# Kernel optimization log

Measured on AMD Instinct MI355X. Metric: run time of the kernel, lower is better.

## Reference

```python
import jax, jax.numpy as jnp
import numpy as np

N, B, M, K, C = 120000, 8, 60000, 16, 32
EX = 512  # 128 * expansion_factor 4
EPS = 1e-5


def _bn(h, g, b):
    # BatchNorm1d (training-mode batch stats, biased var), stats over points
    m = h.mean(axis=0)
    v = h.var(axis=0)
    return (h - m) * jax.lax.rsqrt(v + EPS) * g + b


def setup_inputs() -> dict:
    key = jax.random.key(0)
    ks = jax.random.split(key, 20)

    def w(i, shape, fan):
        return jax.random.normal(ks[i], shape, jnp.float32) / np.sqrt(fan)

    inp = {}
    inp["x"] = jax.random.normal(ks[0], (N, C), jnp.float32)
    inp["pos"] = jax.random.normal(ks[1], (N, 3), jnp.float32) * 5.0
    inp["batch"] = jnp.sort(jax.random.randint(ks[2], (N,), 0, B))
    inp["reflectance"] = jax.random.uniform(ks[3], (N,), jnp.float32)
    inp["sf"] = jax.random.uniform(ks[4], (B,), jnp.float32, minval=0.5, maxval=1.5)
    inp["idx"] = jnp.sort(jax.random.randint(ks[5], (M,), 0, N))
    inp["edge_src"] = jax.random.randint(ks[6], (M * K,), 0, N)
    inp["edge_dst"] = jnp.repeat(jnp.arange(M), K)
    # local_nn MLP channels [C+4, 64, 64, 128]; first layer has no BN
    inp["mlp_W1"] = w(7, (C + 4, 64), C + 4); inp["mlp_b1"] = jnp.zeros((64,))
    inp["mlp_W2"] = w(8, (64, 64), 64); inp["mlp_b2"] = jnp.zeros((64,))
    inp["mlp_g2"] = jnp.ones((64,)); inp["mlp_be2"] = jnp.zeros((64,))
    inp["mlp_W3"] = w(9, (64, 128), 64); inp["mlp_b3"] = jnp.zeros((128,))
    inp["mlp_g3"] = jnp.ones((128,)); inp["mlp_be3"] = jnp.zeros((128,))
    # ReflectanceYesNo (1 -> 32 -> 32 -> 1)
    inp["ryn_W1"] = w(10, (1, 32), 1); inp["ryn_b1"] = jnp.zeros((32,))
    inp["ryn_W2"] = w(11, (32, 32), 32); inp["ryn_b2"] = jnp.zeros((32,))
    inp["ryn_W3"] = w(12, (32, 1), 32); inp["ryn_b3"] = jnp.zeros((1,))
    # InvertedResidualBlock 128 -> 512 -> 128 (all 1x1 convs)
    inp["exp_W"] = w(13, (128, EX), 128); inp["exp_b"] = jnp.zeros((EX,))
    inp["exp_g"] = jnp.ones((EX,)); inp["exp_be"] = jnp.zeros((EX,))
    inp["dw_w"] = jax.random.normal(ks[14], (2, EX), jnp.float32)  # depthwise k=1 -> per-channel scale
    inp["dw_b"] = jnp.zeros((2, EX)); inp["dw_g"] = jnp.ones((2, EX)); inp["dw_be"] = jnp.zeros((2, EX))
    inp["pw_W"] = w(15, (2, EX, EX), EX); inp["pw_b"] = jnp.zeros((2, EX))
    inp["pw_g"] = jnp.ones((2, EX)); inp["pw_be"] = jnp.zeros((2, EX))
    inp["c_g"] = jnp.ones((2, EX)); inp["c_be"] = jnp.zeros((2, EX))
    inp["proj_W"] = w(16, (EX, 128), EX); inp["proj_b"] = jnp.zeros((128,))
    inp["proj_g"] = jnp.ones((128,)); inp["proj_be"] = jnp.zeros((128,))
    return inp


def reference(x, pos, batch, reflectance, sf, idx, edge_src, edge_dst,
              mlp_W1, mlp_b1, mlp_W2, mlp_b2, mlp_g2, mlp_be2, mlp_W3, mlp_b3, mlp_g3, mlp_be3,
              ryn_W1, ryn_b1, ryn_W2, ryn_b2, ryn_W3, ryn_b3,
              exp_W, exp_b, exp_g, exp_be, dw_w, dw_b, dw_g, dw_be,
              pw_W, pw_b, pw_g, pw_be, c_g, c_be, proj_W, proj_b, proj_g, proj_be):
    Bn = sf.shape[0]
    Mn = idx.shape[0]
    pos4 = jnp.concatenate([pos[:, :3], reflectance[:, None]], axis=-1)  # [N,4]

    # --- ReflectanceYesNo gating (gumbel_softmax over a size-1 axis == ones, straight-through) ---
    h = jax.nn.relu(reflectance[:, None] @ ryn_W1 + ryn_b1)
    h = jax.nn.relu(h @ ryn_W2 + ryn_b2)
    pooled = jax.ops.segment_sum(h, batch, num_segments=Bn)
    counts = jax.ops.segment_sum(jnp.ones((h.shape[0],), h.dtype), batch, num_segments=Bn)
    logits = (pooled / counts[:, None]) @ ryn_W3 + ryn_b3  # [B,1]
    y_soft = jax.nn.softmax(logits, axis=-1)               # size-1 softmax -> all ones
    y = jax.lax.stop_gradient(jnp.ones_like(y_soft) - y_soft) + y_soft
    gate = jnp.where(jnp.sum(reflectance) != 0.0, y[:, 0][batch], 1.0)
    refl4 = pos4[:, 3] * gate

    # --- scale coords, PointNetConv: gather -> local_nn MLP -> max aggregate ---
    scale = sf[batch][:, None]
    pos_s = jnp.concatenate([pos4[:, :3] / scale, refl4[:, None]], axis=-1)  # [N,4]
    rel = pos_s[edge_src] - pos_s[idx][edge_dst]                              # [E,4]
    msg = jnp.concatenate([x[edge_src], rel], axis=-1)                        # [E,C+4]
    h1 = jax.nn.relu(msg @ mlp_W1 + mlp_b1)
    h2 = _bn(jax.nn.relu(h1 @ mlp_W2 + mlp_b2), mlp_g2, mlp_be2)
    h3 = _bn(jax.nn.relu(h2 @ mlp_W3 + mlp_b3), mlp_g3, mlp_be3)
    agg = jax.ops.segment_max(h3, edge_dst, num_segments=Mn)                  # [M,128]
    agg = jnp.where(jnp.isneginf(agg), 0.0, agg)  # PyG fills isolated nodes with 0

    # --- InvertedResidualBlock (1x1 convs == per-point linears, BN over points) ---
    res = agg
    e = jax.nn.relu(_bn(agg @ exp_W + exp_b, exp_g, exp_be))

    def ds(hh, i):  # DepthwiseSeparableConv1d, k=1
        d = jax.nn.relu(_bn(hh * dw_w[i] + dw_b[i], dw_g[i], dw_be[i]))
        return jax.nn.relu(_bn(d @ pw_W[i] + pw_b[i], pw_g[i], pw_be[i]))

    cmid = jax.nn.relu(_bn(ds(e, 0), c_g[0], c_be[0]))
    cmid = _bn(ds(cmid, 1), c_g[1], c_be[1])
    o = _bn(cmid @ proj_W + proj_b, proj_g, proj_be)
    out = jax.nn.relu(o + res)  # shortcut is identity (in == out channels)

    return (out, pos[idx, :3], batch[idx], reflectance[idx], sf)
```

## Files before the change

### kernel.cpp

```cpp
#include <hip/hip_runtime.h>
#include <hip/hip_bf16.h>
#include <cstdint>

#define DEV_INLINE __device__ __forceinline__

typedef unsigned short u16;
typedef unsigned int   u32;
typedef short bf16x8 __attribute__((ext_vector_type(8)));
typedef float f32x4  __attribute__((ext_vector_type(4)));

#define AS_GLOBAL(p) ((const __attribute__((address_space(1))) void*)(p))
#define AS_LDS(p)    ((__attribute__((address_space(3))) void*)(p))

constexpr int NP = 120000, NB = 8, NM = 60000, KNN = 16;
constexpr int NE = NM * KNN;
constexpr float EPS = 1e-5f;

constexpr size_t O_POS   = (size_t)NM * 128;
constexpr size_t O_BATCH = O_POS + (size_t)NM * 3;
constexpr size_t O_REFL  = O_BATCH + NM;
constexpr size_t O_SF    = O_REFL + NM;

__device__ float  g_pos_s[(size_t)NP * 4];
__device__ u16    g_xbf[(size_t)NP * 32];
__device__ u16    g_pre2[(size_t)NE * 64];
__device__ u32    g_mm[(size_t)NM * 128];
__device__ float  g_agg[(size_t)NM * 128];
__device__ u16    g_aggbf[(size_t)NM * 128];
__device__ u16    g_bufA[(size_t)NM * 512];
__device__ u16    g_bufB[(size_t)NM * 512];
__device__ float  g_obuf[(size_t)NM * 128];
__device__ float  g_sum[512], g_sqs[512], g_cfa[512], g_cfb[512];
__device__ float  g_b3adj[128], g_pbadj[128];
__device__ u16 g_w1t[64 * 64];
__device__ u16 g_w2t[64 * 64];
__device__ u16 g_w3t[128 * 64];
__device__ u16 g_expwt[512 * 128];
__device__ u16 g_pw0t[512 * 512];
__device__ u16 g_pw1t[512 * 512];
__device__ u16 g_projwt[128 * 512];

template<int ID> DEV_INLINE const u16* ubufsel() {
  if constexpr (ID == 1) return g_aggbf;
  else if constexpr (ID == 2) return g_bufA;
  else return g_bufB;
}
template<int ID> DEV_INLINE u16* obufsel() {
  if constexpr (ID == 2) return g_bufA;
  else return g_bufB;
}
template<int ID> DEV_INLINE const u16* wsel() {
  if constexpr (ID == 3) return g_expwt;
  else if constexpr (ID == 4) return g_pw0t;
  else if constexpr (ID == 5) return g_pw1t;
  else return g_projwt;
}

DEV_INLINE float bf2f(u16 u) { u32 x = (u32)u << 16; float f; __builtin_memcpy(&f, &x, 4); return f; }
DEV_INLINE u16 f2bf(float f) {
  u32 x; __builtin_memcpy(&x, &f, 4);
  return (u16)((x + 0x7FFFu + ((x >> 16) & 1u)) >> 16);
}
DEV_INLINE u32 pack2(float a, float b) { return (u32)f2bf(a) | ((u32)f2bf(b) << 16); }

__global__ void prep_pos_x(const float* __restrict__ pos, const int* __restrict__ batch,
                           const float* __restrict__ refl, const float* __restrict__ sf,
                           const float* __restrict__ x) {
  int i = blockIdx.x * blockDim.x + threadIdx.x;
  if (i >= NP) return;
  float s = sf[batch[i]];
  float4 v;
  v.x = pos[(size_t)i*3+0] / s;
  v.y = pos[(size_t)i*3+1] / s;
  v.z = pos[(size_t)i*3+2] / s;
  v.w = refl[i];
  *reinterpret_cast<float4*>(g_pos_s + (size_t)i*4) = v;
  const float4* xr = reinterpret_cast<const float4*>(x + (size_t)i*32);
#pragma unroll
  for (int q = 0; q < 4; q++) {
    float4 a = xr[q*2], b = xr[q*2+1];
    uint4 u = make_uint4(pack2(a.x,a.y), pack2(a.z,a.w), pack2(b.x,b.y), pack2(b.z,b.w));
    *reinterpret_cast<uint4*>(g_xbf + (size_t)i*32 + q*8) = u;
  }
}

__global__ void tail_out(const float* __restrict__ pos, const int* __restrict__ batch,
                         const float* __restrict__ refl, const float* __restrict__ sf,
                         const int* __restrict__ idx, float* __restrict__ out) {
  int i = blockIdx.x * blockDim.x + threadIdx.x;
  if (i < NM) {
    int p = idx[i];
    out[O_POS + (size_t)i*3+0] = pos[(size_t)p*3+0];
    out[O_POS + (size_t)i*3+1] = pos[(size_t)p*3+1];
    out[O_POS + (size_t)i*3+2] = pos[(size_t)p*3+2];
    out[O_BATCH + i] = (float)batch[p];
    out[O_REFL  + i] = refl[p];
  }
  if (i < NB) out[O_SF + i] = sf[i];
}

__global__ void zero_stats() {
  int t = threadIdx.x;
  g_sum[t] = 0.f; g_sqs[t] = 0.f;
}

__global__ void prep_weights(const float* __restrict__ W1, const float* __restrict__ W2,
                             const float* __restrict__ W3, const float* __restrict__ expW,
                             const float* __restrict__ pwW, const float* __restrict__ projW) {
  int i = blockIdx.x * 256 + threadIdx.x;
  const int s0 = 4096, s1 = 4096, s2 = 8192, s3 = 65536, s4 = 262144, s5 = 262144, s6 = 65536;
  if (i < s0) { int n = i >> 6, k = i & 63; g_w1t[i] = (k < 36) ? f2bf(W1[k*64 + n]) : (u16)0; return; }
  i -= s0;
  if (i < s1) { int n = i >> 6, k = i & 63; g_w2t[i] = f2bf(W2[k*64 + n]); return; }
  i -= s1;
  if (i < s2) { int n = i >> 6, k = i & 63; g_w3t[i] = f2bf(W3[k*128 + n]); return; }
  i -= s2;
  if (i < s3) { int n = i >> 7, k = i & 127; g_expwt[i] = f2bf(expW[k*512 + n]); return; }
  i -= s3;
  if (i < s4) { int n = i >> 9, k = i & 511; g_pw0t[i] = f2bf(pwW[k*512 + n]); return; }
  i -= s4;
  if (i < s5) { int n = i >> 9, k = i & 511; g_pw1t[i] = f2bf(pwW[262144 + k*512 + n]); return; }
  i -= s5;
  if (i < s6) { int n = i >> 9, k = i & 511; g_projwt[i] = f2bf(projW[k*128 + n]); return; }
}

__global__ void param_bn(const float* __restrict__ g, const float* __restrict__ be,
                         float n, int C) {
  int c = threadIdx.x;
  if (c < C) {
    float mean = g_sum[c] / n;
    float var  = fmaxf(g_sqs[c] / n - mean * mean, 0.f);
    float a = g[c] * rsqrtf(var + EPS);
    g_cfa[c] = a;
    g_cfb[c] = be[c] - a * mean;
  }
  __syncthreads();
  g_sum[c] = 0.f; g_sqs[c] = 0.f;
}

__global__ void param_dw(const float* __restrict__ w, const float* __restrict__ g,
                         const float* __restrict__ be, float n, int C) {
  int c = threadIdx.x;
  if (c < C) {
    float mean = g_sum[c] / n;
    float var  = fmaxf(g_sqs[c] / n - mean * mean, 0.f);
    float r = rsqrtf(w[c]*w[c]*var + EPS);
    float a = w[c] * r * g[c];
    g_cfa[c] = a;
    g_cfb[c] = be[c] - a * mean;
  }
  __syncthreads();
  g_sum[c] = 0.f; g_sqs[c] = 0.f;
}

template<int SID>
__global__ void scale_fold(const float* __restrict__ bias_in, int N, int K) {
  u16* Wt = (SID == 0) ? g_w3t : g_projwt;
  float* badj = (SID == 0) ? g_b3adj : g_pbadj;
  int w = (blockIdx.x * blockDim.x + threadIdx.x) >> 6;
  int lane = threadIdx.x & 63;
  if (w >= N) return;
  float acc = 0.f;
  for (int k = lane; k < K; k += 64) {
    float wv = bf2f(Wt[(size_t)w*K + k]);
    acc = fmaf(g_cfb[k], wv, acc);
    Wt[(size_t)w*K + k] = f2bf(g_cfa[k] * wv);
  }
#pragma unroll
  for (int o = 32; o; o >>= 1) acc += __shfl_xor(acc, o, 64);
  if (lane == 0) badj[w] = bias_in[w] + acc;
}

constexpr int K1_BLOCKS = 960;
__launch_bounds__(256)
__global__ void k1_edge(const int* __restrict__ esrc, const int* __restrict__ idx,
                        const float* __restrict__ b1v, const float* __restrict__ b2v) {
  __shared__ u16 sH[4][16][72];
  __shared__ float ssum[64], ssqs[64];
  const int tid = threadIdx.x;
  if (tid < 64) { ssum[tid] = 0.f; ssqs[tid] = 0.f; }
  __syncthreads();
  const int w = tid >> 6, lane = tid & 63, l15 = lane & 15, l4 = lane >> 4;
  u16 (*sh)[72] = sH[w];
  bf16x8 w1f[2][4], w2f[2][4];
#pragma unroll
  for (int ks = 0; ks < 2; ks++)
#pragma unroll
    for (int fc = 0; fc < 4; fc++) {
      w1f[ks][fc] = *reinterpret_cast<const bf16x8*>(g_w1t + (size_t)(fc*16+l15)*64 + ks*32 + l4*8);
      w2f[ks][fc] = *reinterpret_cast<const bf16x8*>(g_w2t + (size_t)(fc*16+l15)*64 + ks*32 + l4*8);
    }
  float b1r[4], b2r[4];
#pragma unroll
  for (int fc = 0; fc < 4; fc++) { b1r[fc] = b1v[fc*16+l15]; b2r[fc] = b2v[fc*16+l15]; }
  float s8[4] = {}, q8[4] = {};
  const int t0 = blockIdx.x * 4 + w;
  const int TSTRIDE = K1_BLOCKS * 4;
  int   s_cur = esrc[t0*16 + l15];
  uint4 x_cur = *reinterpret_cast<const uint4*>(g_xbf + (size_t)s_cur*32 + l4*8);
  float4 ps_cur = make_float4(0.f,0.f,0.f,0.f);
  if (l4 == 0) ps_cur = *reinterpret_cast<const float4*>(g_pos_s + (size_t)s_cur*4);
  float4 pc_cur = *reinterpret_cast<const float4*>(g_pos_s + (size_t)idx[t0]*4);

  for (int t = t0; t < NM; t += TSTRIDE) {
    const int tn = t + TSTRIDE;
    int s_nx = 0; uint4 x_nx = make_uint4(0,0,0,0);
    float4 ps_nx = ps_cur, pc_nx = pc_cur;
    if (tn < NM) {
      s_nx = esrc[tn*16 + l15];
      x_nx = *reinterpret_cast<const uint4*>(g_xbf + (size_t)s_nx*32 + l4*8);
      if (l4 == 0) ps_nx = *reinterpret_cast<const float4*>(g_pos_s + (size_t)s_nx*4);
      pc_nx = *reinterpret_cast<const float4*>(g_pos_s + (size_t)idx[tn]*4);
    }
    bf16x8 a0 = __builtin_bit_cast(bf16x8, x_cur);
    uint4 r4 = make_uint4(0,0,0,0);
    if (l4 == 0) {
      r4.x = pack2(ps_cur.x - pc_cur.x, ps_cur.y - pc_cur.y);
      r4.y = pack2(ps_cur.z - pc_cur.z, ps_cur.w - pc_cur.w);
    }
    bf16x8 a1 = __builtin_bit_cast(bf16x8, r4);
    f32x4 acc1[4] = {};
#pragma unroll
    for (int fc = 0; fc < 4; fc++) {
      acc1[fc] = __builtin_amdgcn_mfma_f32_16x16x32_bf16(a0, w1f[0][fc], acc1[fc], 0, 0, 0);
      acc1[fc] = __builtin_amdgcn_mfma_f32_16x16x32_bf16(a1, w1f[1][fc], acc1[fc], 0, 0, 0);
    }
#pragma unroll
    for (int fc = 0; fc < 4; fc++)
#pragma unroll
      for (int r = 0; r < 4; r++)
        sh[l4*4 + r][fc*16 + l15] = f2bf(fmaxf(acc1[fc][r] + b1r[fc], 0.f));
    bf16x8 h0  = *reinterpret_cast<const bf16x8*>(&sh[l15][l4*8]);
    bf16x8 h1v = *reinterpret_cast<const bf16x8*>(&sh[l15][32 + l4*8]);
    f32x4 acc2[4] = {};
#pragma unroll
    for (int fc = 0; fc < 4; fc++) {
      acc2[fc] = __builtin_amdgcn_mfma_f32_16x16x32_bf16(h0,  w2f[0][fc], acc2[fc], 0, 0, 0);
      acc2[fc] = __builtin_amdgcn_mfma_f32_16x16x32_bf16(h1v, w2f[1][fc], acc2[fc], 0, 0, 0);
    }
#pragma unroll
    for (int fc = 0; fc < 4; fc++)
#pragma unroll
      for (int r = 0; r < 4; r++) {
        float v = fmaxf(acc2[fc][r] + b2r[fc], 0.f);
        s8[fc] += v; q8[fc] += v*v;
        sh[l4*4 + r][fc*16 + l15] = f2bf(v);
      }
    uint4 p0 = *reinterpret_cast<const uint4*>(&sh[l15][l4*8]);
    uint4 p1 = *reinterpret_cast<const uint4*>(&sh[l15][32 + l4*8]);
    *reinterpret_cast<uint4*>(g_pre2 + (size_t)t*1024 + lane*8)       = p0;
    *reinterpret_cast<uint4*>(g_pre2 + (size_t)t*1024 + 512 + lane*8) = p1;
    s_cur = s_nx; x_cur = x_nx; ps_cur = ps_nx; pc_cur = pc_nx;
  }
#pragma unroll
  for (int fc = 0; fc < 4; fc++) {
    float sv = s8[fc], qv = q8[fc];
    sv += __shfl_xor(sv, 16, 64); sv += __shfl_xor(sv, 32, 64);
    qv += __shfl_xor(qv, 16, 64); qv += __shfl_xor(qv, 32, 64);
    if (l4 == 0) { atomicAdd(&ssum[fc*16 + l15], sv); atomicAdd(&ssqs[fc*16 + l15], qv); }
  }
  __syncthreads();
  if (tid < 64) { atomicAdd(&g_sum[tid], ssum[tid]); atomicAdd(&g_sqs[tid], ssqs[tid]); }
}

constexpr int K2_BLOCKS = 960;
__launch_bounds__(256)
__global__ void k2_edge() {
  __shared__ float ssum[128], ssqs[128];
  const int tid = threadIdx.x;
  if (tid < 128) { ssum[tid] = 0.f; ssqs[tid] = 0.f; }
  __syncthreads();
  const int lane = tid & 63, l15 = lane & 15, l4 = lane >> 4;
  const int wglobal = blockIdx.x * 4 + (tid >> 6);
  const int WSTRIDE = K2_BLOCKS * 4;
  bf16x8 w3f[2][8];
#pragma unroll
  for (int ks = 0; ks < 2; ks++)
#pragma unroll
    for (int fc = 0; fc < 8; fc++)
      w3f[ks][fc] = *reinterpret_cast<const bf16x8*>(g_w3t + (size_t)(fc*16 + l15)*64 + ks*32 + l4*8);
  float bv[8];
#pragma unroll
  for (int fc = 0; fc < 8; fc++) bv[fc] = g_b3adj[fc*16 + l15];
  float s[8] = {}, q[8] = {};
  int t = wglobal;
  uint4 an0 = make_uint4(0,0,0,0), an1 = an0;
  if (t < NM) {
    const uint4* p = reinterpret_cast<const uint4*>(g_pre2 + (size_t)t*1024 + lane*8);
    an0 = p[0]; an1 = p[64];
  }
  for (; t < NM; t += WSTRIDE) {
    uint4 a0 = an0, a1 = an1;
    int tn = t + WSTRIDE;
    if (tn < NM) {
      const uint4* p = reinterpret_cast<const uint4*>(g_pre2 + (size_t)tn*1024 + lane*8);
      an0 = p[0]; an1 = p[64];
    }
    bf16x8 af0 = __builtin_bit_cast(bf16x8, a0);
    bf16x8 af1 = __builtin_bit_cast(bf16x8, a1);
    f32x4 acc[8] = {};
#pragma unroll
    for (int fc = 0; fc < 8; fc++) {
      acc[fc] = __builtin_amdgcn_mfma_f32_16x16x32_bf16(af0, w3f[0][fc], acc[fc], 0, 0, 0);
      acc[fc] = __builtin_amdgcn_mfma_f32_16x16x32_bf16(af1, w3f[1][fc], acc[fc], 0, 0, 0);
    }
    u32 rbase = (u32)t * 128u;
#pragma unroll
    for (int fc = 0; fc < 8; fc++) {
      float v0 = fmaxf(acc[fc][0] + bv[fc], 0.f);
      float v1 = fmaxf(acc[fc][1] + bv[fc], 0.f);
      float v2 = fmaxf(acc[fc][2] + bv[fc], 0.f);
      float v3 = fmaxf(acc[fc][3] + bv[fc], 0.f);
      s[fc] += (v0 + v1) + (v2 + v3);
      q[fc] += (v0*v0 + v1*v1) + (v2*v2 + v3*v3);
      float mx = fmaxf(fmaxf(v0, v1), fmaxf(v2, v3));
      float mn = fminf(fminf(v0, v1), fminf(v2, v3));
      mx = fmaxf(mx, __shfl_xor(mx, 16, 64)); mx = fmaxf(mx, __shfl_xor(mx, 32, 64));
      mn = fminf(mn, __shfl_xor(mn, 16, 64)); mn = fminf(mn, __shfl_xor(mn, 32, 64));
      if (l4 == (fc & 3))
        g_mm[rbase + fc*16 + l15] = (u32)f2bf(mx) | ((u32)f2bf(mn) << 16);
    }
  }
#pragma unroll
  for (int fc = 0; fc < 8; fc++) {
    float sv = s[fc], qv = q[fc];
    sv += __shfl_xor(sv, 16, 64); sv += __shfl_xor(sv, 32, 64);
    qv += __shfl_xor(qv, 16, 64); qv += __shfl_xor(qv, 32, 64);
    if (l4 == 0) { atomicAdd(&ssum[fc*16 + l15], sv); atomicAdd(&ssqs[fc*16 + l15], qv); }
  }
  __syncthreads();
  if (tid < 128) { atomicAdd(&g_sum[tid], ssum[tid]); atomicAdd(&g_sqs[tid], ssqs[tid]); }
}

__global__ void k3_agg() {
  int i4 = (blockIdx.x * 256 + threadIdx.x) * 4;
  if (i4 >= NM * 128) return;
  int c = i4 & 127;
  uint4 mm = *reinterpret_cast<const uint4*>(g_mm + i4);
  float4 a = *reinterpret_cast<const float4*>(g_cfa + c);
  float4 b = *reinterpret_cast<const float4*>(g_cfb + c);
  u32 u[4] = {mm.x, mm.y, mm.z, mm.w};
  float av[4] = {a.x, a.y, a.z, a.w};
  float bb[4] = {b.x, b.y, b.z, b.w};
  float4 r;
  float* rr = &r.x;
#pragma unroll
  for (int j = 0; j < 4; j++) {
    float mx = bf2f((u16)(u[j] & 0xFFFFu));
    float mn = bf2f((u16)(u[j] >> 16));
    rr[j] = av[j] > 0.f ? fmaf(av[j], mx, bb[j]) : fmaf(av[j], mn, bb[j]);
  }
  *reinterpret_cast<float4*>(g_agg + i4) = r;
  uint2 pk; pk.x = pack2(r.x, r.y); pk.y = pack2(r.z, r.w);
  *reinterpret_cast<uint2*>(g_aggbf + i4) = pk;
}

template<int AID, int WID, int OID, int NPAN, bool OUT_BF16, bool BIAS_DEV>
__launch_bounds__(256, 3)
__global__ void gemm_mfma(const float* __restrict__ bias, int Mrows, int Kdim) {
  const int Ncols = NPAN * 128;
  const u16* __restrict__ A  = ubufsel<AID>();
  const u16* __restrict__ Bt = wsel<WID>();
  __shared__ u16 As[2][128][32];
  __shared__ u16 Bs[2][128][32];
  __shared__ float ssum[128], ssqs[128];
  const int tid = threadIdx.x;
  const int bid = blockIdx.x;
  const int m0 = (bid / NPAN) * 128, n0 = (bid % NPAN) * 128;
  if (tid < 128) { ssum[tid] = 0.f; ssqs[tid] = 0.f; }
  const int wave = tid >> 6, lane = tid & 63, l15 = lane & 15, l4 = lane >> 4;
  const int wr = wave >> 1, wc = wave & 1;
  const int ckk = (lane & 3) * 8;
  f32x4 acc[4][4] = {};
  const int nt = Kdim >> 5;

  auto STAGE = [&](int buf, int t) {
    const int k0 = t * 32;
#pragma unroll
    for (int i = 0; i < 2; i++) {
      const int c = wave * 2 + i;
      const int row = c * 16 + (lane >> 2);
      const u16* ga = A  + (size_t)(m0 + row) * Kdim + k0 + ckk;
      const u16* gb = Bt + (size_t)(n0 + row) * Kdim + k0 + ckk;
      __builtin_amdgcn_global_load_lds(AS_GLOBAL(ga), AS_LDS(&As[buf][c*16][0]), 16, 0, 0);
      __builtin_amdgcn_global_load_lds(AS_GLOBAL(gb), AS_LDS(&Bs[buf][c*16][0]), 16, 0, 0);
    }
  };

  STAGE(0, 0);
  __syncthreads();
  int cur = 0;
  for (int t = 0; t < nt; ++t) {
    if (t + 1 < nt) STAGE(cur ^ 1, t + 1);
    bf16x8 af[4], bf[4];
#pragma unroll
    for (int fr = 0; fr < 4; fr++)
      af[fr] = *reinterpret_cast<const bf16x8*>(&As[cur][wr*64 + fr*16 + l15][l4*8]);
#pragma unroll
    for (int fc = 0; fc < 4; fc++)
      bf[fc] = *reinterpret_cast<const bf16x8*>(&Bs[cur][wc*64 + fc*16 + l15][l4*8]);
#pragma unroll
    for (int fr = 0; fr < 4; fr++)
#pragma unroll
      for (int fc = 0; fc < 4; fc++)
        acc[fr][fc] = __builtin_amdgcn_mfma_f32_16x16x32_bf16(af[fr], bf[fc], acc[fr][fc], 0, 0, 0);
    if (t + 1 < nt) { __syncthreads(); cur ^= 1; }
  }

  const int orow = m0 + wr*64 + l4*4;
#pragma unroll
  for (int fc = 0; fc < 4; fc++) {
    int col = n0 + wc*64 + fc*16 + l15;
    float bvv = BIAS_DEV ? g_pbadj[col] : bias[col];
    float s = 0.f, q = 0.f;
#pragma unroll
    for (int fr = 0; fr < 4; fr++)
#pragma unroll
      for (int r = 0; r < 4; r++) {
        int row = orow + fr*16 + r;
        if (row < Mrows) {
          float v = acc[fr][fc][r] + bvv;
          s += v; q += v*v;
          if (OUT_BF16) obufsel<OID>()[(size_t)row*Ncols + col] = f2bf(v);
          else          g_obuf[(size_t)row*Ncols + col] = v;
        }
      }
    atomicAdd(&ssum[wc*64 + fc*16 + l15], s);
    atomicAdd(&ssqs[wc*64 + fc*16 + l15], q);
  }
  __syncthreads();
  if (tid < 128) { atomicAdd(&g_sum[n0 + tid], ssum[tid]); atomicAdd(&g_sqs[n0 + tid], ssqs[tid]); }
}

template<int INID, int OUTID>
__launch_bounds__(256)
__global__ void ew_stats(int rows) {
  const u16* __restrict__ X = ubufsel<INID>();
  u16* __restrict__ Y = obufsel<OUTID>();
  __shared__ float ssum[512], ssqs[512];
  const int tid = threadIdx.x;
  ssum[tid] = 0.f; ssum[tid+256] = 0.f; ssqs[tid] = 0.f; ssqs[tid+256] = 0.f;
  __syncthreads();
  const int c0 = (tid & 63) * 8;
  const int rl = tid >> 6;
  float a[8], b[8];
#pragma unroll
  for (int j = 0; j < 8; j++) { a[j] = g_cfa[c0+j]; b[j] = g_cfb[c0+j]; }
  float s[8] = {}, q[8] = {};
  for (int r = blockIdx.x*4 + rl; r < rows; r += gridDim.x*4) {
    uint4 v = *reinterpret_cast<const uint4*>(X + (size_t)r*512 + c0);
    u32 u[4] = {v.x, v.y, v.z, v.w}, o[4];
#pragma unroll
    for (int t = 0; t < 4; t++) {
      float lo = bf2f((u16)(u[t] & 0xFFFFu));
      float hi = bf2f((u16)(u[t] >> 16));
      lo = fmaxf(fmaf(a[2*t],   lo, b[2*t]),   0.f);
      hi = fmaxf(fmaf(a[2*t+1], hi, b[2*t+1]), 0.f);
      s[2*t] += lo; q[2*t] += lo*lo; s[2*t+1] += hi; q[2*t+1] += hi*hi;
      o[t] = (u32)f2bf(lo) | ((u32)f2bf(hi) << 16);
    }
    *reinterpret_cast<uint4*>(Y + (size_t)r*512 + c0) = make_uint4(o[0], o[1], o[2], o[3]);
  }
#pragma unroll
  for (int j = 0; j < 8; j++) { atomicAdd(&ssum[c0+j], s[j]); atomicAdd(&ssqs[c0+j], q[j]); }
  __syncthreads();
  atomicAdd(&g_sum[tid],     ssum[tid]);     atomicAdd(&g_sqs[tid],     ssqs[tid]);
  atomicAdd(&g_sum[tid+256], ssum[tid+256]); atomicAdd(&g_sqs[tid+256], ssqs[tid+256]);
}

template<int INID, int OUTID>
__launch_bounds__(256)
__global__ void ew_apply(int rows) {
  const u16* __restrict__ X = ubufsel<INID>();
  u16* __restrict__ Y = obufsel<OUTID>();
  const int tid = threadIdx.x;
  const int c0 = (tid & 63) * 8;
  const int rl = tid >> 6;
  float a[8], b[8];
#pragma unroll
  for (int j = 0; j < 8; j++) { a[j] = g_cfa[c0+j]; b[j] = g_cfb[c0+j]; }
  for (int r = blockIdx.x*4 + rl; r < rows; r += gridDim.x*4) {
    uint4 v = *reinterpret_cast<const uint4*>(X + (size_t)r*512 + c0);
    u32 u[4] = {v.x, v.y, v.z, v.w}, o[4];
#pragma unroll
    for (int t = 0; t < 4; t++) {
      float lo = bf2f((u16)(u[t] & 0xFFFFu));
      float hi = bf2f((u16)(u[t] >> 16));
      lo = fmaxf(fmaf(a[2*t],   lo, b[2*t]),   0.f);
      hi = fmaxf(fmaf(a[2*t+1], hi, b[2*t+1]), 0.f);
      o[t] = (u32)f2bf(lo) | ((u32)f2bf(hi) << 16);
    }
    *reinterpret_cast<uint4*>(Y + (size_t)r*512 + c0) = make_uint4(o[0], o[1], o[2], o[3]);
  }
}

__global__ void final_out(float* __restrict__ out) {
  int i4 = (blockIdx.x * 256 + threadIdx.x) * 4;
  if (i4 >= NM * 128) return;
  int c = i4 & 127;
  float4 o  = *reinterpret_cast<const float4*>(g_obuf + i4);
  float4 ag = *reinterpret_cast<const float4*>(g_agg + i4);
  float4 a  = *reinterpret_cast<const float4*>(g_cfa + c);
  float4 b  = *reinterpret_cast<const float4*>(g_cfb + c);
  float4 r;
  r.x = fmaxf(fmaf(a.x, o.x, b.x) + ag.x, 0.f);
  r.y = fmaxf(fmaf(a.y, o.y, b.y) + ag.y, 0.f);
  r.z = fmaxf(fmaf(a.z, o.z, b.z) + ag.z, 0.f);
  r.w = fmaxf(fmaf(a.w, o.w, b.w) + ag.w, 0.f);
  *reinterpret_cast<float4*>(out + i4) = r;
}

extern "C" void kernel_launch(void* const* d_in, const int* in_sizes, int n_in,
                              void* d_out, int out_size, void* d_ws, size_t ws_size,
                              hipStream_t stream) {
  const float* x     = (const float*)d_in[0];
  const float* pos   = (const float*)d_in[1];
  const int*   batch = (const int*)  d_in[2];
  const float* refl  = (const float*)d_in[3];
  const float* sf    = (const float*)d_in[4];
  const int*   idx   = (const int*)  d_in[5];
  const int*   esrc  = (const int*)  d_in[6];
  const float* W1  = (const float*)d_in[8];
  const float* b1  = (const float*)d_in[9];
  const float* W2  = (const float*)d_in[10];
  const float* b2  = (const float*)d_in[11];
  const float* g2  = (const float*)d_in[12];
  const float* be2 = (const float*)d_in[13];
  const float* W3  = (const float*)d_in[14];
  const float* b3  = (const float*)d_in[15];
  const float* g3  = (const float*)d_in[16];
  const float* be3 = (const float*)d_in[17];
  const float* expW  = (const float*)d_in[24];
  const float* expb  = (const float*)d_in[25];
  const float* expg  = (const float*)d_in[26];
  const float* expbe = (const float*)d_in[27];
  const float* dww  = (const float*)d_in[28];
  const float* dwg  = (const float*)d_in[30];
  const float* dwbe = (const float*)d_in[31];
  const float* pwW  = (const float*)d_in[32];
  const float* pwb  = (const float*)d_in[33];
  const float* pwg  = (const float*)d_in[34];
  const float* pwbe = (const float*)d_in[35];
  const float* cg   = (const float*)d_in[36];
  const float* cbe  = (const float*)d_in[37];
  const float* projW  = (const float*)d_in[38];
  const float* projb  = (const float*)d_in[39];
  const float* projg  = (const float*)d_in[40];
  const float* projbe = (const float*)d_in[41];
  float* out = (float*)d_out;

  const float fNE = (float)NE, fNM = (float)NM;

  prep_weights<<<2624, 256, 0, stream>>>(W1, W2, W3, expW, pwW, projW);
  prep_pos_x<<<(NP + 255)/256, 256, 0, stream>>>(pos, batch, refl, sf, x);
  tail_out<<<(NM + 255)/256, 256, 0, stream>>>(pos, batch, refl, sf, idx, out);
  zero_stats<<<1, 512, 0, stream>>>();

  k1_edge<<<K1_BLOCKS, 256, 0, stream>>>(esrc, idx, b1, b2);
  param_bn<<<1, 512, 0, stream>>>(g2, be2, fNE, 64);
  scale_fold<0><<<32, 256, 0, stream>>>(b3, 128, 64);
  k2_edge<<<K2_BLOCKS, 256, 0, stream>>>();
  param_bn<<<1, 512, 0, stream>>>(g3, be3, fNE, 128);
  k3_agg<<<NM*128/1024, 256, 0, stream>>>();

  gemm_mfma<1, 3, 2, 4, true, false><<<469*4, 256, 0, stream>>>(expb, NM, 128);
  param_bn<<<1, 512, 0, stream>>>(expg, expbe, fNM, 512);
  ew_stats<2, 2><<<1024, 256, 0, stream>>>(NM);
  param_dw<<<1, 512, 0, stream>>>(dww, dwg, dwbe, fNM, 512);
  ew_apply<2, 3><<<1024, 256, 0, stream>>>(NM);
  gemm_mfma<3, 4, 2, 4, true, false><<<469*4, 256, 0, stream>>>(pwb, NM, 512);
  param_bn<<<1, 512, 0, stream>>>(pwg, pwbe, fNM, 512);
  ew_stats<2, 2><<<1024, 256, 0, stream>>>(NM);
  param_bn<<<1, 512, 0, stream>>>(cg, cbe, fNM, 512);
  ew_stats<2, 2><<<1024, 256, 0, stream>>>(NM);
  param_dw<<<1, 512, 0, stream>>>(dww + 512, dwg + 512, dwbe + 512, fNM, 512);
  ew_apply<2, 3><<<1024, 256, 0, stream>>>(NM);
  gemm_mfma<3, 5, 2, 4, true, false><<<469*4, 256, 0, stream>>>(pwb + 512, NM, 512);
  param_bn<<<1, 512, 0, stream>>>(pwg + 512, pwbe + 512, fNM, 512);
  ew_stats<2, 2><<<1024, 256, 0, stream>>>(NM);
  param_bn<<<1, 512, 0, stream>>>(cg + 512, cbe + 512, fNM, 512);
  scale_fold<1><<<32, 256, 0, stream>>>(projb, 128, 512);
  gemm_mfma<2, 6, 0, 1, false, true><<<469, 256, 0, stream>>>(projb, NM, 512);
  param_bn<<<1, 512, 0, stream>>>(projg, projbe, fNM, 128);
  final_out<<<NM*128/1024, 256, 0, stream>>>(out);
}
```

Baseline: 828.0 us.

## Stage bf16 GEMM output through LDS for coalesced stores, clamp A rows

The MFMA GEMM's bf16 epilogue now writes the tile into the reused LDS staging buffer, then copies whole rows to global memory with 16-byte vector stores. This replaces the scattered 2-byte per-element stores. Out-of-range A rows are clamped during staging, and the occupancy hint rises from 3 to 4 blocks per CU. The cost is an extra barrier and an LDS round trip, plus possible register pressure from the tighter launch bound.

```diff
diff --git a/kernel.cpp b/kernel.cpp
--- a/kernel.cpp
+++ b/kernel.cpp
@@ -356,14 +356,15 @@
 }
 
 template<int AID, int WID, int OID, int NPAN, bool OUT_BF16, bool BIAS_DEV>
-__launch_bounds__(256, 3)
+__launch_bounds__(256, 4)
 __global__ void gemm_mfma(const float* __restrict__ bias, int Mrows, int Kdim) {
   const int Ncols = NPAN * 128;
   const u16* __restrict__ A  = ubufsel<AID>();
   const u16* __restrict__ Bt = wsel<WID>();
-  __shared__ u16 As[2][128][32];
-  __shared__ u16 Bs[2][128][32];
+  __shared__ u16 sLDS[16384];
   __shared__ float ssum[128], ssqs[128];
+  u16* sA = sLDS;
+  u16* sB = sLDS + 8192;
   const int tid = threadIdx.x;
   const int bid = blockIdx.x;
   const int m0 = (bid / NPAN) * 128, n0 = (bid % NPAN) * 128;
@@ -379,11 +380,13 @@
 #pragma unroll
     for (int i = 0; i < 2; i++) {
       const int c = wave * 2 + i;
-      const int row = c * 16 + (lane >> 2);
-      const u16* ga = A  + (size_t)(m0 + row) * Kdim + k0 + ckk;
-      const u16* gb = Bt + (size_t)(n0 + row) * Kdim + k0 + ckk;
-      __builtin_amdgcn_global_load_lds(AS_GLOBAL(ga), AS_LDS(&As[buf][c*16][0]), 16, 0, 0);
-      __builtin_amdgcn_global_load_lds(AS_GLOBAL(gb), AS_LDS(&Bs[buf][c*16][0]), 16, 0, 0);
+      int ar = m0 + c * 16 + (lane >> 2);
+      if (ar >= Mrows) ar = Mrows - 1;
+      const int br = n0 + c * 16 + (lane >> 2);
+      __builtin_amdgcn_global_load_lds(AS_GLOBAL(A  + (size_t)ar * Kdim + k0 + ckk),
+                                       AS_LDS(sA + buf*4096 + c*512), 16, 0, 0);
+      __builtin_amdgcn_global_load_lds(AS_GLOBAL(Bt + (size_t)br * Kdim + k0 + ckk),
+                                       AS_LDS(sB + buf*4096 + c*512), 16, 0, 0);
     }
   };
 
@@ -392,21 +395,26 @@
   int cur = 0;
   for (int t = 0; t < nt; ++t) {
     if (t + 1 < nt) STAGE(cur ^ 1, t + 1);
-    bf16x8 af[4], bf[4];
+    bf16x8 af[4], bf4[4];
+#pragma unroll
+    for (int fr = 0; fr < 4; fr++) {
+      int r = wr*64 + fr*16 + l15;
+      af[fr] = *reinterpret_cast<const bf16x8*>(sA + cur*4096 + r*32 + l4*8);
+    }
+#pragma unroll
+    for (int fc = 0; fc < 4; fc++) {
+      int r = wc*64 + fc*16 + l15;
+      bf4[fc] = *reinterpret_cast<const bf16x8*>(sB + cur*4096 + r*32 + l4*8);
+    }
 #pragma unroll
     for (int fr = 0; fr < 4; fr++)
-      af[fr] = *reinterpret_cast<const bf16x8*>(&As[cur][wr*64 + fr*16 + l15][l4*8]);
-#pragma unroll
-    for (int fc = 0; fc < 4; fc++)
-      bf[fc] = *reinterpret_cast<const bf16x8*>(&Bs[cur][wc*64 + fc*16 + l15][l4*8]);
-#pragma unroll
-    for (int fr = 0; fr < 4; fr++)
 #pragma unroll
       for (int fc = 0; fc < 4; fc++)
-        acc[fr][fc] = __builtin_amdgcn_mfma_f32_16x16x32_bf16(af[fr], bf[fc], acc[fr][fc], 0, 0, 0);
+        acc[fr][fc] = __builtin_amdgcn_mfma_f32_16x16x32_bf16(af[fr], bf4[fc], acc[fr][fc], 0, 0, 0);
     if (t + 1 < nt) { __syncthreads(); cur ^= 1; }
   }
 
+  __syncthreads();
   const int orow = m0 + wr*64 + l4*4;
 #pragma unroll
   for (int fc = 0; fc < 4; fc++) {
@@ -421,7 +429,7 @@
         if (row < Mrows) {
           float v = acc[fr][fc][r] + bvv;
           s += v; q += v*v;
-          if (OUT_BF16) obufsel<OID>()[(size_t)row*Ncols + col] = f2bf(v);
+          if (OUT_BF16) sLDS[(size_t)(wr*64 + fr*16 + l4*4 + r)*128 + wc*64 + fc*16 + l15] = f2bf(v);
           else          g_obuf[(size_t)row*Ncols + col] = v;
         }
       }
@@ -429,6 +437,15 @@
     atomicAdd(&ssqs[wc*64 + fc*16 + l15], q);
   }
   __syncthreads();
+  if (OUT_BF16) {
+    const int r2 = tid >> 1, hh = tid & 1;
+    if (m0 + r2 < Mrows) {
+      const uint4* src = reinterpret_cast<const uint4*>(sLDS + r2*128 + hh*64);
+      uint4* dst = reinterpret_cast<uint4*>(obufsel<OID>() + (size_t)(m0 + r2)*Ncols + n0 + hh*64);
+#pragma unroll
+      for (int j = 0; j < 8; j++) dst[j] = src[j];
+    }
+  }
   if (tid < 128) { atomicAdd(&g_sum[n0 + tid], ssum[tid]); atomicAdd(&g_sqs[n0 + tid], ssqs[tid]); }
 }
 
```

After: 708.4 us. 1.17x faster.
